# Kernel tuning notes

Measured on AMD Instinct MI355X. Metric: run time of the kernel, lower is better.

## Reference

```python
import jax, jax.numpy as jnp
import numpy as np

B, T, E = 2, 2048, 2048
H, HKV, DH = 16, 8, 128
G = H // HKV
WINDOW = 512
ROPE_THETA = 10000.0
EPS = 1e-6


def _rms_norm(x, w):
    # Gemma3RMSNorm: fp32 rms_norm with weight = 1 + w
    xf = x.astype(jnp.float32)
    y = xf * jax.lax.rsqrt(jnp.mean(xf * xf, axis=-1, keepdims=True) + EPS)
    return (y * (1.0 + w.astype(jnp.float32))).astype(x.dtype)


def _rotate_half(x):
    x1, x2 = x[..., : DH // 2], x[..., DH // 2 :]
    return jnp.concatenate((-x2, x1), axis=-1)


def setup_inputs() -> dict:
    key = jax.random.key(0)
    ks = jax.random.split(key, 5)
    s = 0.02
    return {
        "x": jax.random.normal(ks[0], (B, T, E), jnp.float32),
        "wq": jax.random.normal(ks[1], (H * DH, E), jnp.float32) * s,
        "wk": jax.random.normal(ks[2], (HKV * DH, E), jnp.float32) * s,
        "wv": jax.random.normal(ks[3], (HKV * DH, E), jnp.float32) * s,
        "wo": jax.random.normal(ks[4], (E, H * DH), jnp.float32) * s,
        "q_norm_w": jnp.zeros((DH,), jnp.float32),
        "k_norm_w": jnp.zeros((DH,), jnp.float32),
    }


def reference(x, wq, wk, wv, wo, q_norm_w, k_norm_w):
    # projections: [B,T,H,DH] -> [B,H,T,DH]
    q = (x @ wq.T).reshape(B, T, H, DH).transpose(0, 2, 1, 3)
    k = (x @ wk.T).reshape(B, T, HKV, DH).transpose(0, 2, 1, 3)
    v = (x @ wv.T).reshape(B, T, HKV, DH).transpose(0, 2, 1, 3)

    # QK-RMSNorm over head_dim
    q = _rms_norm(q, q_norm_w)
    k = _rms_norm(k, k_norm_w)

    # RoPE (prefill: positions 0..T-1)
    pos = jnp.arange(T, dtype=jnp.float32)
    inv_freq = 1.0 / (ROPE_THETA ** (jnp.arange(0, DH, 2, dtype=jnp.float32) / DH))
    freqs = pos[:, None] * inv_freq[None, :]          # [T, DH//2]
    emb = jnp.concatenate((freqs, freqs), axis=-1)    # [T, DH]
    cos = jnp.cos(emb)[None, None, :, :]
    sin = jnp.sin(emb)[None, None, :, :]
    q = q * cos + _rotate_half(q) * sin
    k = k * cos + _rotate_half(k) * sin

    # GQA attention with causal + sliding-window mask, fp32 scores
    q = q * (DH ** -0.5)
    qg = q.reshape(B, HKV, G, T, DH)
    att = jnp.einsum("bhgtd,bhkd->bhgtk", qg.astype(jnp.float32), k.astype(jnp.float32))

    dist = jnp.arange(T)[:, None] - jnp.arange(T)[None, :]   # [T, T]
    mask = (dist >= 0) & (dist <= WINDOW)
    att = jnp.where(mask[None, None, None, :, :], att, jnp.finfo(jnp.float32).min)
    att = jax.nn.softmax(att, axis=-1).astype(q.dtype)

    ctx = jnp.einsum("bhgtk,bhkd->bhgtd", att, v)
    out = ctx.reshape(B, H, T, DH).transpose(0, 2, 1, 3).reshape(B, T, H * DH)
    return out @ wo.T
```

## Files before the change

### kernel.cpp

```cpp
#include <hip/hip_runtime.h>
#include <hip/hip_bf16.h>
#include <stdint.h>

#define B_ 2
#define T_ 2048
#define E_ 2048
#define H_ 16
#define HKV_ 8
#define DH_ 128
#define WINDOW_ 512

typedef unsigned short ush;
typedef float f32x4 __attribute__((ext_vector_type(4)));
typedef __bf16 bf16x8 __attribute__((ext_vector_type(8)));
typedef uint32_t u32x4 __attribute__((ext_vector_type(4)));

static __device__ __forceinline__ ush f2bf(float f) {
    uint32_t u = __float_as_uint(f);
    uint32_t r = (u + 0x7fffu + ((u >> 16) & 1u)) >> 16;
    return (ush)r;
}
static __device__ __forceinline__ float bf2f(ush h) {
    return __uint_as_float(((uint32_t)h) << 16);
}

__global__ __launch_bounds__(256) void cast_all(const float* __restrict__ x,
        const float* __restrict__ wq, const float* __restrict__ wk,
        const float* __restrict__ wv, const float* __restrict__ wo,
        ush* __restrict__ dst) {
    const int stride = gridDim.x * blockDim.x;
    for (int i = blockIdx.x * blockDim.x + threadIdx.x; i < 5242880; i += stride) {
        const float4* src;
        if (i < 2097152)      src = (const float4*)x  + i;
        else if (i < 3145728) src = (const float4*)wq + (i - 2097152);
        else if (i < 3670016) src = (const float4*)wk + (i - 3145728);
        else if (i < 4194304) src = (const float4*)wv + (i - 3670016);
        else                  src = (const float4*)wo + (i - 4194304);
        const float4 f = *src;
        ushort4 o;
        o.x = f2bf(f.x); o.y = f2bf(f.y); o.z = f2bf(f.z); o.w = f2bf(f.w);
        reinterpret_cast<ushort4*>(dst)[i] = o;
    }
}

template <int MODE>
__global__ __launch_bounds__(512, 2) void gemm_bt3(
    const ush* __restrict__ A, const ush* __restrict__ Bm,
    float* __restrict__ Cf, ush* __restrict__ q, ush* __restrict__ k, ush* __restrict__ vT,
    int M, int N, int K)
{
    __shared__ ush As[3][128 * 64];
    __shared__ ush Bs[3][256 * 64];
    const int tid = threadIdx.x;
    const int lane = tid & 63;
    const int wid = tid >> 6;
    const int wr = wid >> 2, wc = wid & 3;
    const int g = lane >> 4, t = lane & 15;
    const int gm0 = blockIdx.x * 128, gn0 = blockIdx.y * 256;

    f32x4 acc[4][4] = {};

    auto stageA2 = [&](int kt, int m3) {
#pragma unroll
        for (int i = 0; i < 2; ++i) {
            const int C = i * 512 + tid;
            const int r = C >> 3, c = C & 7;
            const ush* src = A + (size_t)(gm0 + r) * K + (kt << 6) + ((c ^ (r & 7)) << 3);
            __builtin_amdgcn_global_load_lds(
                (const __attribute__((address_space(1))) void*)src,
                (__attribute__((address_space(3))) void*)(&As[m3][C << 3]), 16, 0, 0);
        }
    };
    auto stageB4 = [&](int kt, int m3) {
#pragma unroll
        for (int i = 0; i < 4; ++i) {
            const int C = i * 512 + tid;
            const int r = C >> 3, c = C & 7;
            const ush* src = Bm + (size_t)(gn0 + r) * K + (kt << 6) + ((c ^ (r & 7)) << 3);
            __builtin_amdgcn_global_load_lds(
                (const __attribute__((address_space(1))) void*)src,
                (__attribute__((address_space(3))) void*)(&Bs[m3][C << 3]), 16, 0, 0);
        }
    };

    const int nt = K >> 6;

    stageA2(0, 0); stageB4(0, 0);
    stageA2(1, 1); stageB4(1, 1);
    asm volatile("s_waitcnt vmcnt(6)" ::: "memory");
    __builtin_amdgcn_s_barrier();
    __builtin_amdgcn_sched_barrier(0);

    int m3 = 0;
    for (int kt = 0; kt < nt; ++kt) {
        const int st3 = (m3 + 2 >= 3) ? m3 - 1 : m3 + 2;
        bf16x8 af[4][2], bfr[4][2];

#pragma unroll
        for (int mf = 0; mf < 4; ++mf)
#pragma unroll
            for (int ks = 0; ks < 2; ++ks) {
                const int row = wr * 64 + mf * 16 + t;
                af[mf][ks] = *reinterpret_cast<const bf16x8*>(
                    &As[m3][row * 64 + ((((ks << 2) + g) ^ (t & 7)) << 3)]);
            }
#pragma unroll
        for (int nf = 0; nf < 4; ++nf)
#pragma unroll
            for (int ks = 0; ks < 2; ++ks) {
                const int row = wc * 64 + nf * 16 + t;
                bfr[nf][ks] = *reinterpret_cast<const bf16x8*>(
                    &Bs[m3][row * 64 + ((((ks << 2) + g) ^ (t & 7)) << 3)]);
            }

        if (kt + 2 < nt) { stageA2(kt + 2, st3); stageB4(kt + 2, st3); }

        __builtin_amdgcn_s_setprio(1);
#pragma unroll
        for (int ks = 0; ks < 2; ++ks)
#pragma unroll
            for (int mf = 0; mf < 4; ++mf)
#pragma unroll
                for (int nf = 0; nf < 4; ++nf)
                    acc[mf][nf] = __builtin_amdgcn_mfma_f32_16x16x32_bf16(
                        af[mf][ks], bfr[nf][ks], acc[mf][nf], 0, 0, 0);
        __builtin_amdgcn_s_setprio(0);

        if (kt + 1 < nt) {
            if (kt + 2 < nt) asm volatile("s_waitcnt vmcnt(6)" ::: "memory");
            else             asm volatile("s_waitcnt vmcnt(0)" ::: "memory");
        }
        __builtin_amdgcn_s_barrier();
        __builtin_amdgcn_sched_barrier(0);

        m3 = (m3 + 1 >= 3) ? 0 : m3 + 1;
    }

    const int rsub = (lane >> 4) << 2;
    const int csub = lane & 15;
#pragma unroll
    for (int mf = 0; mf < 4; ++mf) {
        const int row0 = gm0 + wr * 64 + mf * 16 + rsub;
#pragma unroll
        for (int nf = 0; nf < 4; ++nf) {
            const int col = gn0 + wc * 64 + nf * 16 + csub;
#pragma unroll
            for (int r = 0; r < 4; ++r) {
                const int row = row0 + r;
                if (MODE == 1) {
                    Cf[(size_t)row * N + col] = acc[mf][nf][r];
                } else {
                    const int bb = row >> 11, tt = row & (T_ - 1);
                    const ush val = f2bf(acc[mf][nf][r]);
                    if (col < H_ * DH_) {
                        const int hh = col >> 7, d = col & 127;
                        q[((((size_t)bb * H_ + hh) * T_ + tt) << 7) + d] = val;
                    } else if (col < H_ * DH_ + HKV_ * DH_) {
                        const int c2 = col - H_ * DH_;
                        const int hh = c2 >> 7, d = c2 & 127;
                        k[((((size_t)bb * HKV_ + hh) * T_ + tt) << 7) + d] = val;
                    } else {
                        const int c2 = col - H_ * DH_ - HKV_ * DH_;
                        const int hh = c2 >> 7, d = c2 & 127;
                        vT[((size_t)((bb * HKV_ + hh) * DH_ + d) << 11) + tt] = val;
                    }
                }
            }
        }
    }
}

__global__ __launch_bounds__(256) void norm_rope(ush* __restrict__ q, ush* __restrict__ k,
                                                 const float* __restrict__ qw,
                                                 const float* __restrict__ kw)
{
    const int lane = threadIdx.x & 63;
    const int row = blockIdx.x * 4 + (threadIdx.x >> 6);
    const int NQ = B_ * H_ * T_;
    ush* p; const float* w; int t; bool isq = (row < NQ);
    if (isq) { p = q + ((size_t)row << 7); t = row & (T_ - 1); w = qw; }
    else     { int r2 = row - NQ; p = k + ((size_t)r2 << 7); t = r2 & (T_ - 1); w = kw; }

    float x0 = bf2f(p[lane]);
    float x1 = bf2f(p[lane + 64]);
    float ss = x0 * x0 + x1 * x1;
#pragma unroll
    for (int off = 32; off; off >>= 1) ss += __shfl_xor(ss, off);
    const float rms = rsqrtf(ss * (1.0f / 128.0f) + 1e-6f);
    float y0 = x0 * rms * (1.0f + w[lane]);
    float y1 = x1 * rms * (1.0f + w[lane + 64]);

    const float invf = expf(-(float)lane * 0.14391156831212787f);
    const float fr = (float)t * invf;
    const float c = cosf(fr), s = sinf(fr);
    float o0 = y0 * c - y1 * s;
    float o1 = y1 * c + y0 * s;
    if (isq) { o0 *= 0.08838834764831845f; o1 *= 0.08838834764831845f; }
    p[lane] = f2bf(o0);
    p[lane + 64] = f2bf(o1);
}

__global__ __launch_bounds__(256) void attn_mfma(const ush* __restrict__ q,
        const ush* __restrict__ k, const ush* __restrict__ vT, ush* __restrict__ ctx)
{
    __shared__ ush Ks[2][32 * 128];
    __shared__ ush Vs[2][128 * 32];
    const int tid = threadIdx.x;
    const int lane = tid & 63;
    const int w = tid >> 6;
    const int g = lane >> 4;
    const int t = lane & 15;

    int bi = blockIdx.x;
    bi = (bi & 7) * 128 + (bi >> 3);
    const int qtile = bi & 31;
    const int hh = (bi >> 5) & 15;
    const int b = bi >> 9;
    const int qb = qtile * 64;
    const int hkv = hh >> 1;

    const ush* qptr = q + ((((size_t)b * H_ + hh) * T_ + qb) << 7);
    const ush* kbase = k + (((size_t)b * HKV_ + hkv) << 18);
    const ush* vtbase = vT + (((size_t)b * HKV_ + hkv) << 18);

    bf16x8 qf[4];
#pragma unroll
    for (int c = 0; c < 4; ++c)
        qf[c] = *reinterpret_cast<const bf16x8*>(qptr + ((16 * w + t) << 7) + 32 * c + 8 * g);

    const int kstart = (qb >= WINDOW_) ? (qb - WINDOW_) : 0;
    const int nt = (qb + 64 - kstart) >> 5;

    auto stage = [&](int ti, int buf) {
        const int kt0 = kstart + (ti << 5);
#pragma unroll
        for (int i = 0; i < 2; ++i) {
            const int C = w * 128 + i * 64 + lane;
            {
                const int row = C >> 4, ch = C & 15;
                const ush* gk = kbase + ((size_t)(kt0 + row) << 7) + ch * 8;
                __builtin_amdgcn_global_load_lds(
                    (const __attribute__((address_space(1))) void*)gk,
                    (__attribute__((address_space(3))) void*)(&Ks[buf][(w * 128 + i * 64) * 8]),
                    16, 0, 0);
            }
            {
                const int row = C >> 2, ch = C & 3;
                const ush* gv = vtbase + ((size_t)row << 11) + kt0 + ch * 8;
                __builtin_amdgcn_global_load_lds(
                    (const __attribute__((address_space(1))) void*)gv,
                    (__attribute__((address_space(3))) void*)(&Vs[buf][(w * 128 + i * 64) * 8]),
                    16, 0, 0);
            }
        }
    };

    float m = -1e30f, lsum = 0.f;
    f32x4 o[8] = {};

    stage(0, 0);
    __syncthreads();

    for (int ti = 0; ti < nt; ++ti) {
        const int cur = ti & 1;
        if (ti + 1 < nt) stage(ti + 1, cur ^ 1);
        const int kt0 = kstart + (ti << 5);
        const int qw0 = qb + 16 * w;
        const bool active = (kt0 + 31 >= qw0 - WINDOW_) && (kt0 <= qw0 + 15);
        if (active) {
            f32x4 st[2] = {};
#pragma unroll
            for (int s = 0; s < 2; ++s)
#pragma unroll
                for (int c = 0; c < 4; ++c) {
                    bf16x8 kf = *reinterpret_cast<const bf16x8*>(
                        &Ks[cur][(16 * s + t) * 128 + 32 * c + 8 * g]);
                    st[s] = __builtin_amdgcn_mfma_f32_16x16x32_bf16(kf, qf[c], st[s], 0, 0, 0);
                }
            const int tg = qb + 16 * w + t;
            float e[2][4];
            float mymax = -3e38f;
#pragma unroll
            for (int s = 0; s < 2; ++s)
#pragma unroll
                for (int r = 0; r < 4; ++r) {
                    const int key = kt0 + 16 * s + 4 * g + r;
                    const int dist = tg - key;
                    const bool valid = (dist >= 0) && (dist <= WINDOW_);
                    const float sv = valid ? st[s][r] : -3e38f;
                    e[s][r] = sv;
                    mymax = fmaxf(mymax, sv);
                }
            mymax = fmaxf(mymax, __shfl_xor(mymax, 16));
            mymax = fmaxf(mymax, __shfl_xor(mymax, 32));
            const float mn = fmaxf(m, mymax);
            const float sc = __expf(m - mn);
            float esum = 0.f;
#pragma unroll
            for (int s = 0; s < 2; ++s)
#pragma unroll
                for (int r = 0; r < 4; ++r) {
                    const float ev = __expf(e[s][r] - mn);
                    e[s][r] = ev;
                    esum += ev;
                }
            esum += __shfl_xor(esum, 16);
            esum += __shfl_xor(esum, 32);
            lsum = lsum * sc + esum;
            m = mn;
#pragma unroll
            for (int ds = 0; ds < 8; ++ds) {
                o[ds][0] *= sc; o[ds][1] *= sc; o[ds][2] *= sc; o[ds][3] *= sc;
            }
            uint32_t word[2][2];
#pragma unroll
            for (int s = 0; s < 2; ++s)
#pragma unroll
                for (int wd = 0; wd < 2; ++wd)
                    word[s][wd] = (uint32_t)f2bf(e[s][2 * wd])
                                | ((uint32_t)f2bf(e[s][2 * wd + 1]) << 16);
            u32x4 bw;
#pragma unroll
            for (int e2 = 0; e2 < 4; ++e2) {
                const int srcl = 16 * (2 * (g & 1) + (e2 >> 1)) + t;
                const uint32_t v0 = __shfl(word[0][e2 & 1], srcl);
                const uint32_t v1 = __shfl(word[1][e2 & 1], srcl);
                bw[e2] = (g >= 2) ? v1 : v0;
            }
            const bf16x8 pF = __builtin_bit_cast(bf16x8, bw);
#pragma unroll
            for (int ds = 0; ds < 8; ++ds) {
                bf16x8 vtF = *reinterpret_cast<const bf16x8*>(
                    &Vs[cur][(16 * ds + t) * 32 + 8 * g]);
                o[ds] = __builtin_amdgcn_mfma_f32_16x16x32_bf16(vtF, pF, o[ds], 0, 0, 0);
            }
        }
        __syncthreads();
    }

    const float linv = 1.0f / lsum;
    ush* cptr = ctx + (((size_t)b * T_ + qb + 16 * w + t) * (H_ * DH_)) + hh * DH_;
#pragma unroll
    for (int ds = 0; ds < 8; ++ds) {
        ushort4 pk;
        pk.x = f2bf(o[ds][0] * linv);
        pk.y = f2bf(o[ds][1] * linv);
        pk.z = f2bf(o[ds][2] * linv);
        pk.w = f2bf(o[ds][3] * linv);
        *reinterpret_cast<ushort4*>(cptr + 16 * ds + 4 * g) = pk;
    }
}

extern "C" void kernel_launch(void* const* d_in, const int* in_sizes, int n_in,
                              void* d_out, int out_size, void* d_ws, size_t ws_size,
                              hipStream_t stream)
{
    const float* x   = (const float*)d_in[0];
    const float* wq  = (const float*)d_in[1];
    const float* wk  = (const float*)d_in[2];
    const float* wv  = (const float*)d_in[3];
    const float* wo  = (const float*)d_in[4];
    const float* qnw = (const float*)d_in[5];
    const float* knw = (const float*)d_in[6];
    float* out = (float*)d_out;

    ush* ws    = (ush*)d_ws;
    ush* xbf   = ws;
    ush* wqkv  = xbf  + 8388608;
    ush* wobf  = wqkv + 8388608;
    ush* qraw  = wobf + 4194304;
    ush* kraw  = qraw + 8388608;
    ush* vTb   = kraw + 4194304;
    ush* ctx   = vTb  + 4194304;

    cast_all<<<2048, 256, 0, stream>>>(x, wq, wk, wv, wo, ws);

    gemm_bt3<0><<<dim3(32, 16), 512, 0, stream>>>(xbf, wqkv, nullptr, qraw, kraw, vTb,
                                                  4096, 4096, 2048);
    norm_rope<<<(65536 + 32768) / 4, 256, 0, stream>>>(qraw, kraw, qnw, knw);
    attn_mfma<<<1024, 256, 0, stream>>>(qraw, kraw, vTb, ctx);
    gemm_bt3<1><<<dim3(32, 8), 512, 0, stream>>>(ctx, wobf, out, nullptr, nullptr, nullptr,
                                                 4096, 2048, 2048);
    (void)in_sizes; (void)n_in; (void)out_size; (void)ws_size;
}
```

Baseline: 236.8 us.

## Switch GEMMs to 32x32x16 MFMA with BK=32 and 4-stage pipeline

Rewrites the bf16 GEMM kernel to use 32x32x16 MFMA instructions with a K-step of 32, a four-buffer LDS ring (three stages in flight), and a new XOR swizzle. The QKV projection now uses 256x256 block tiles (M_REP=4), half as many blocks, while the output projection keeps 128x256. The goal is fewer LDS reads per MFMA and more reuse per block, at the cost of more accumulator registers and a longer, more intricate vmcnt wait schedule.

```diff
diff --git a/kernel.cpp b/kernel.cpp
--- a/kernel.cpp
+++ b/kernel.cpp
@@ -12,6 +12,7 @@
 
 typedef unsigned short ush;
 typedef float f32x4 __attribute__((ext_vector_type(4)));
+typedef float f32x16 __attribute__((ext_vector_type(16)));
 typedef __bf16 bf16x8 __attribute__((ext_vector_type(8)));
 typedef uint32_t u32x4 __attribute__((ext_vector_type(4)));
 
@@ -43,115 +44,118 @@
     }
 }
 
-template <int MODE>
-__global__ __launch_bounds__(512, 2) void gemm_bt3(
+template <int M_REP, int MODE>
+__global__ __launch_bounds__(512, 2) void gemm_bt4(
     const ush* __restrict__ A, const ush* __restrict__ Bm,
     float* __restrict__ Cf, ush* __restrict__ q, ush* __restrict__ k, ush* __restrict__ vT,
     int M, int N, int K)
 {
-    __shared__ ush As[3][128 * 64];
-    __shared__ ush Bs[3][256 * 64];
+    __shared__ ush As[4][M_REP * 64 * 32];
+    __shared__ ush Bs[4][256 * 32];
     const int tid = threadIdx.x;
     const int lane = tid & 63;
     const int wid = tid >> 6;
     const int wr = wid >> 2, wc = wid & 3;
-    const int g = lane >> 4, t = lane & 15;
-    const int gm0 = blockIdx.x * 128, gn0 = blockIdx.y * 256;
-
-    f32x4 acc[4][4] = {};
-
-    auto stageA2 = [&](int kt, int m3) {
+    const int l31 = lane & 31, lh = lane >> 5;
+    const int gm0 = blockIdx.x * (M_REP * 64), gn0 = blockIdx.y * 256;
+
+    f32x16 acc[M_REP][2] = {};
+
+    auto stage = [&](int kt, int buf) {
+#pragma unroll
+        for (int i = 0; i < M_REP / 2; ++i) {
+            const int C = i * 512 + tid;
+            const int r = C >> 2, c = C & 3;
+            const ush* src = A + (size_t)(gm0 + r) * K + (kt << 5)
+                             + ((c ^ ((r >> 1) & 3)) << 3);
+            __builtin_amdgcn_global_load_lds(
+                (const __attribute__((address_space(1))) void*)src,
+                (__attribute__((address_space(3))) void*)(&As[buf][C << 3]), 16, 0, 0);
+        }
 #pragma unroll
         for (int i = 0; i < 2; ++i) {
             const int C = i * 512 + tid;
-            const int r = C >> 3, c = C & 7;
-            const ush* src = A + (size_t)(gm0 + r) * K + (kt << 6) + ((c ^ (r & 7)) << 3);
+            const int r = C >> 2, c = C & 3;
+            const ush* src = Bm + (size_t)(gn0 + r) * K + (kt << 5)
+                             + ((c ^ ((r >> 1) & 3)) << 3);
             __builtin_amdgcn_global_load_lds(
                 (const __attribute__((address_space(1))) void*)src,
-                (__attribute__((address_space(3))) void*)(&As[m3][C << 3]), 16, 0, 0);
+                (__attribute__((address_space(3))) void*)(&Bs[buf][C << 3]), 16, 0, 0);
         }
     };
-    auto stageB4 = [&](int kt, int m3) {
-#pragma unroll
-        for (int i = 0; i < 4; ++i) {
-            const int C = i * 512 + tid;
-            const int r = C >> 3, c = C & 7;
-            const ush* src = Bm + (size_t)(gn0 + r) * K + (kt << 6) + ((c ^ (r & 7)) << 3);
-            __builtin_amdgcn_global_load_lds(
-                (const __attribute__((address_space(1))) void*)src,
-                (__attribute__((address_space(3))) void*)(&Bs[m3][C << 3]), 16, 0, 0);
-        }
-    };
-
-    const int nt = K >> 6;
-
-    stageA2(0, 0); stageB4(0, 0);
-    stageA2(1, 1); stageB4(1, 1);
-    asm volatile("s_waitcnt vmcnt(6)" ::: "memory");
+
+    const int nt = K >> 5;
+
+    stage(0, 0); stage(1, 1); stage(2, 2);
+    if constexpr (M_REP == 4) asm volatile("s_waitcnt vmcnt(8)" ::: "memory");
+    else                      asm volatile("s_waitcnt vmcnt(6)" ::: "memory");
     __builtin_amdgcn_s_barrier();
     __builtin_amdgcn_sched_barrier(0);
 
-    int m3 = 0;
-    for (int kt = 0; kt < nt; ++kt) {
-        const int st3 = (m3 + 2 >= 3) ? m3 - 1 : m3 + 2;
-        bf16x8 af[4][2], bfr[4][2];
-
-#pragma unroll
-        for (int mf = 0; mf < 4; ++mf)
-#pragma unroll
-            for (int ks = 0; ks < 2; ++ks) {
-                const int row = wr * 64 + mf * 16 + t;
+    for (int t = 0; t < nt; ++t) {
+        const int buf = t & 3;
+        bf16x8 af[M_REP][2], bfr[2][2];
+
+#pragma unroll
+        for (int mf = 0; mf < M_REP; ++mf) {
+            const int row = wr * (M_REP * 32) + mf * 32 + l31;
+            const int sw = (row >> 1) & 3;
+#pragma unroll
+            for (int ks = 0; ks < 2; ++ks)
                 af[mf][ks] = *reinterpret_cast<const bf16x8*>(
-                    &As[m3][row * 64 + ((((ks << 2) + g) ^ (t & 7)) << 3)]);
-            }
-#pragma unroll
-        for (int nf = 0; nf < 4; ++nf)
-#pragma unroll
-            for (int ks = 0; ks < 2; ++ks) {
-                const int row = wc * 64 + nf * 16 + t;
+                    &As[buf][row * 32 + (((ks * 2 + lh) ^ sw) << 3)]);
+        }
+#pragma unroll
+        for (int nf = 0; nf < 2; ++nf) {
+            const int row = wc * 64 + nf * 32 + l31;
+            const int sw = (row >> 1) & 3;
+#pragma unroll
+            for (int ks = 0; ks < 2; ++ks)
                 bfr[nf][ks] = *reinterpret_cast<const bf16x8*>(
-                    &Bs[m3][row * 64 + ((((ks << 2) + g) ^ (t & 7)) << 3)]);
-            }
-
-        if (kt + 2 < nt) { stageA2(kt + 2, st3); stageB4(kt + 2, st3); }
+                    &Bs[buf][row * 32 + (((ks * 2 + lh) ^ sw) << 3)]);
+        }
+
+        if (t + 3 < nt) stage(t + 3, (t + 3) & 3);
 
         __builtin_amdgcn_s_setprio(1);
 #pragma unroll
         for (int ks = 0; ks < 2; ++ks)
 #pragma unroll
-            for (int mf = 0; mf < 4; ++mf)
-#pragma unroll
-                for (int nf = 0; nf < 4; ++nf)
-                    acc[mf][nf] = __builtin_amdgcn_mfma_f32_16x16x32_bf16(
+            for (int mf = 0; mf < M_REP; ++mf)
+#pragma unroll
+                for (int nf = 0; nf < 2; ++nf)
+                    acc[mf][nf] = __builtin_amdgcn_mfma_f32_32x32x16_bf16(
                         af[mf][ks], bfr[nf][ks], acc[mf][nf], 0, 0, 0);
         __builtin_amdgcn_s_setprio(0);
 
-        if (kt + 1 < nt) {
-            if (kt + 2 < nt) asm volatile("s_waitcnt vmcnt(6)" ::: "memory");
-            else             asm volatile("s_waitcnt vmcnt(0)" ::: "memory");
+        if (t + 3 < nt) {
+            if constexpr (M_REP == 4) asm volatile("s_waitcnt vmcnt(8)" ::: "memory");
+            else                      asm volatile("s_waitcnt vmcnt(6)" ::: "memory");
+        } else if (t + 2 < nt) {
+            if constexpr (M_REP == 4) asm volatile("s_waitcnt vmcnt(4)" ::: "memory");
+            else                      asm volatile("s_waitcnt vmcnt(3)" ::: "memory");
+        } else if (t + 1 < nt) {
+            asm volatile("s_waitcnt vmcnt(0)" ::: "memory");
         }
         __builtin_amdgcn_s_barrier();
         __builtin_amdgcn_sched_barrier(0);
-
-        m3 = (m3 + 1 >= 3) ? 0 : m3 + 1;
-    }
-
-    const int rsub = (lane >> 4) << 2;
-    const int csub = lane & 15;
-#pragma unroll
-    for (int mf = 0; mf < 4; ++mf) {
-        const int row0 = gm0 + wr * 64 + mf * 16 + rsub;
-#pragma unroll
-        for (int nf = 0; nf < 4; ++nf) {
-            const int col = gn0 + wc * 64 + nf * 16 + csub;
-#pragma unroll
-            for (int r = 0; r < 4; ++r) {
-                const int row = row0 + r;
+    }
+
+#pragma unroll
+    for (int mf = 0; mf < M_REP; ++mf) {
+        const int rbase = gm0 + wr * (M_REP * 32) + mf * 32 + 4 * lh;
+#pragma unroll
+        for (int nf = 0; nf < 2; ++nf) {
+            const int col = gn0 + wc * 64 + nf * 32 + l31;
+#pragma unroll
+            for (int r = 0; r < 16; ++r) {
+                const int row = rbase + (r & 3) + 8 * (r >> 2);
+                const float v = acc[mf][nf][r];
                 if (MODE == 1) {
-                    Cf[(size_t)row * N + col] = acc[mf][nf][r];
+                    Cf[(size_t)row * N + col] = v;
                 } else {
                     const int bb = row >> 11, tt = row & (T_ - 1);
-                    const ush val = f2bf(acc[mf][nf][r]);
+                    const ush val = f2bf(v);
                     if (col < H_ * DH_) {
                         const int hh = col >> 7, d = col & 127;
                         q[((((size_t)bb * H_ + hh) * T_ + tt) << 7) + d] = val;
@@ -375,11 +379,11 @@
 
     cast_all<<<2048, 256, 0, stream>>>(x, wq, wk, wv, wo, ws);
 
-    gemm_bt3<0><<<dim3(32, 16), 512, 0, stream>>>(xbf, wqkv, nullptr, qraw, kraw, vTb,
-                                                  4096, 4096, 2048);
+    gemm_bt4<4, 0><<<dim3(16, 16), 512, 0, stream>>>(xbf, wqkv, nullptr, qraw, kraw, vTb,
+                                                     4096, 4096, 2048);
     norm_rope<<<(65536 + 32768) / 4, 256, 0, stream>>>(qraw, kraw, qnw, knw);
     attn_mfma<<<1024, 256, 0, stream>>>(qraw, kraw, vTb, ctx);
-    gemm_bt3<1><<<dim3(32, 8), 512, 0, stream>>>(ctx, wobf, out, nullptr, nullptr, nullptr,
-                                                 4096, 2048, 2048);
+    gemm_bt4<2, 1><<<dim3(32, 8), 512, 0, stream>>>(ctx, wobf, out, nullptr, nullptr, nullptr,
+                                                    4096, 2048, 2048);
     (void)in_sizes; (void)n_in; (void)out_size; (void)ws_size;
 }
```

New measurement: 248.2 us. 4.8% more time.

## Replace triple-buffered GEMM with double-buffered ping-pong phases and larger QKV tile

Applied to the files above, without the earlier changes.

Rewrites the bf16 GEMM to use two LDS buffers instead of three. The main loop is split into phases over pairs of M-fragments, with barriers between phases so waves interleave LDS reads and MFMA work. The tile height becomes a template parameter: the QKV projection uses 256x256 tiles (half as many blocks) and the output projection keeps 128x256. The aim is better operand reuse and a schedule closer to the hipBLASLt ping-pong style. In exchange it exposes more load latency because only one tile is prefetched, and it adds extra barriers.

```diff
diff --git a/kernel.cpp b/kernel.cpp
--- a/kernel.cpp
+++ b/kernel.cpp
@@ -43,35 +43,36 @@
     }
 }
 
-template <int MODE>
-__global__ __launch_bounds__(512, 2) void gemm_bt3(
+template <int MF, int MODE>
+__global__ __launch_bounds__(512, 2) void gemm_bt5(
     const ush* __restrict__ A, const ush* __restrict__ Bm,
     float* __restrict__ Cf, ush* __restrict__ q, ush* __restrict__ k, ush* __restrict__ vT,
     int M, int N, int K)
 {
-    __shared__ ush As[3][128 * 64];
-    __shared__ ush Bs[3][256 * 64];
+    constexpr int BM = MF * 32;
+    __shared__ ush As[2][BM * 64];
+    __shared__ ush Bs[2][256 * 64];
     const int tid = threadIdx.x;
     const int lane = tid & 63;
     const int wid = tid >> 6;
     const int wr = wid >> 2, wc = wid & 3;
     const int g = lane >> 4, t = lane & 15;
-    const int gm0 = blockIdx.x * 128, gn0 = blockIdx.y * 256;
-
-    f32x4 acc[4][4] = {};
-
-    auto stageA2 = [&](int kt, int m3) {
-#pragma unroll
-        for (int i = 0; i < 2; ++i) {
+    const int gm0 = blockIdx.x * BM, gn0 = blockIdx.y * 256;
+
+    f32x4 acc[MF][4] = {};
+
+    auto stageA = [&](int kt, int buf) {
+#pragma unroll
+        for (int i = 0; i < BM / 64; ++i) {
             const int C = i * 512 + tid;
             const int r = C >> 3, c = C & 7;
             const ush* src = A + (size_t)(gm0 + r) * K + (kt << 6) + ((c ^ (r & 7)) << 3);
             __builtin_amdgcn_global_load_lds(
                 (const __attribute__((address_space(1))) void*)src,
-                (__attribute__((address_space(3))) void*)(&As[m3][C << 3]), 16, 0, 0);
+                (__attribute__((address_space(3))) void*)(&As[buf][C << 3]), 16, 0, 0);
         }
     };
-    auto stageB4 = [&](int kt, int m3) {
+    auto stageB = [&](int kt, int buf) {
 #pragma unroll
         for (int i = 0; i < 4; ++i) {
             const int C = i * 512 + tid;
@@ -79,68 +80,66 @@
             const ush* src = Bm + (size_t)(gn0 + r) * K + (kt << 6) + ((c ^ (r & 7)) << 3);
             __builtin_amdgcn_global_load_lds(
                 (const __attribute__((address_space(1))) void*)src,
-                (__attribute__((address_space(3))) void*)(&Bs[m3][C << 3]), 16, 0, 0);
+                (__attribute__((address_space(3))) void*)(&Bs[buf][C << 3]), 16, 0, 0);
         }
     };
 
     const int nt = K >> 6;
 
-    stageA2(0, 0); stageB4(0, 0);
-    stageA2(1, 1); stageB4(1, 1);
-    asm volatile("s_waitcnt vmcnt(6)" ::: "memory");
+    stageA(0, 0); stageB(0, 0);
+    asm volatile("s_waitcnt vmcnt(0)" ::: "memory");
     __builtin_amdgcn_s_barrier();
     __builtin_amdgcn_sched_barrier(0);
 
-    int m3 = 0;
     for (int kt = 0; kt < nt; ++kt) {
-        const int st3 = (m3 + 2 >= 3) ? m3 - 1 : m3 + 2;
-        bf16x8 af[4][2], bfr[4][2];
-
-#pragma unroll
-        for (int mf = 0; mf < 4; ++mf)
-#pragma unroll
-            for (int ks = 0; ks < 2; ++ks) {
-                const int row = wr * 64 + mf * 16 + t;
-                af[mf][ks] = *reinterpret_cast<const bf16x8*>(
-                    &As[m3][row * 64 + ((((ks << 2) + g) ^ (t & 7)) << 3)]);
-            }
-#pragma unroll
-        for (int nf = 0; nf < 4; ++nf)
-#pragma unroll
-            for (int ks = 0; ks < 2; ++ks) {
-                const int row = wc * 64 + nf * 16 + t;
-                bfr[nf][ks] = *reinterpret_cast<const bf16x8*>(
-                    &Bs[m3][row * 64 + ((((ks << 2) + g) ^ (t & 7)) << 3)]);
-            }
-
-        if (kt + 2 < nt) { stageA2(kt + 2, st3); stageB4(kt + 2, st3); }
-
-        __builtin_amdgcn_s_setprio(1);
-#pragma unroll
-        for (int ks = 0; ks < 2; ++ks)
-#pragma unroll
-            for (int mf = 0; mf < 4; ++mf)
+        const int cur = kt & 1;
+        bf16x8 bfr[4][2];
+
+#pragma unroll
+        for (int p = 0; p < MF / 2; ++p) {
+            bf16x8 af[2][2];
+#pragma unroll
+            for (int mm = 0; mm < 2; ++mm)
+#pragma unroll
+                for (int ks = 0; ks < 2; ++ks) {
+                    const int row = wr * (MF * 16) + (2 * p + mm) * 16 + t;
+                    af[mm][ks] = *reinterpret_cast<const bf16x8*>(
+                        &As[cur][row * 64 + ((((ks << 2) + g) ^ (t & 7)) << 3)]);
+                }
+            if (p == 0) {
 #pragma unroll
                 for (int nf = 0; nf < 4; ++nf)
-                    acc[mf][nf] = __builtin_amdgcn_mfma_f32_16x16x32_bf16(
-                        af[mf][ks], bfr[nf][ks], acc[mf][nf], 0, 0, 0);
-        __builtin_amdgcn_s_setprio(0);
-
-        if (kt + 1 < nt) {
-            if (kt + 2 < nt) asm volatile("s_waitcnt vmcnt(6)" ::: "memory");
-            else             asm volatile("s_waitcnt vmcnt(0)" ::: "memory");
-        }
-        __builtin_amdgcn_s_barrier();
-        __builtin_amdgcn_sched_barrier(0);
-
-        m3 = (m3 + 1 >= 3) ? 0 : m3 + 1;
+#pragma unroll
+                    for (int ks = 0; ks < 2; ++ks) {
+                        const int row = wc * 64 + nf * 16 + t;
+                        bfr[nf][ks] = *reinterpret_cast<const bf16x8*>(
+                            &Bs[cur][row * 64 + ((((ks << 2) + g) ^ (t & 7)) << 3)]);
+                    }
+                if (kt + 1 < nt) { stageA(kt + 1, cur ^ 1); stageB(kt + 1, cur ^ 1); }
+            }
+            __builtin_amdgcn_s_barrier();
+            __builtin_amdgcn_s_setprio(1);
+#pragma unroll
+            for (int ks = 0; ks < 2; ++ks)
+#pragma unroll
+                for (int mm = 0; mm < 2; ++mm)
+#pragma unroll
+                    for (int nf = 0; nf < 4; ++nf)
+                        acc[2 * p + mm][nf] = __builtin_amdgcn_mfma_f32_16x16x32_bf16(
+                            af[mm][ks], bfr[nf][ks], acc[2 * p + mm][nf], 0, 0, 0);
+            __builtin_amdgcn_s_setprio(0);
+            if (p == MF / 2 - 1 && kt + 1 < nt)
+                asm volatile("s_waitcnt vmcnt(0)" ::: "memory");
+            __builtin_amdgcn_s_barrier();
+            __builtin_amdgcn_sched_barrier(0);
+        }
     }
 
     const int rsub = (lane >> 4) << 2;
     const int csub = lane & 15;
 #pragma unroll
-    for (int mf = 0; mf < 4; ++mf) {
-        const int row0 = gm0 + wr * 64 + mf * 16 + rsub;
+    for (int mf = 0; mf < MF; ++mf) {
+        const int row0 = gm0 + wr * (MF * 16) + mf * 16 + rsub;
 #pragma unroll
         for (int nf = 0; nf < 4; ++nf) {
             const int col = gn0 + wc * 64 + nf * 16 + csub;
@@ -375,11 +374,11 @@
 
     cast_all<<<2048, 256, 0, stream>>>(x, wq, wk, wv, wo, ws);
 
-    gemm_bt3<0><<<dim3(32, 16), 512, 0, stream>>>(xbf, wqkv, nullptr, qraw, kraw, vTb,
-                                                  4096, 4096, 2048);
+    gemm_bt5<8, 0><<<dim3(16, 16), 512, 0, stream>>>(xbf, wqkv, nullptr, qraw, kraw, vTb,
+                                                     4096, 4096, 2048);
     norm_rope<<<(65536 + 32768) / 4, 256, 0, stream>>>(qraw, kraw, qnw, knw);
     attn_mfma<<<1024, 256, 0, stream>>>(qraw, kraw, vTb, ctx);
-    gemm_bt3<1><<<dim3(32, 8), 512, 0, stream>>>(ctx, wobf, out, nullptr, nullptr, nullptr,
-                                                 4096, 2048, 2048);
+    gemm_bt5<4, 1><<<dim3(32, 8), 512, 0, stream>>>(ctx, wobf, out, nullptr, nullptr, nullptr,
+                                                    4096, 2048, 2048);
     (void)in_sizes; (void)n_in; (void)out_size; (void)ws_size;
 }
```

Measured after the change: 236.0 us. About the same (-0.3%).

## Shrink GEMM tiles to 128x128 with double buffering and swizzled block order

Applied to the files above, without the earlier changes.

The GEMM kernel changes from 128x256 tiles with a 3-stage LDS pipeline to 128x128 tiles with 2-stage double buffering. Launch bounds now allow 4 blocks per CU, and a block-index swizzle groups tiles for L2 reuse. The aim is more blocks in flight and better occupancy on the CUs, at the cost of less data reuse per tile, a shallower prefetch pipeline and a full vmcnt(0) wait every iteration.

```diff
diff --git a/kernel.cpp b/kernel.cpp
--- a/kernel.cpp
+++ b/kernel.cpp
@@ -44,23 +44,28 @@
 }
 
 template <int MODE>
-__global__ __launch_bounds__(512, 2) void gemm_bt3(
+__global__ __launch_bounds__(512, 4) void gemm_bt6(
     const ush* __restrict__ A, const ush* __restrict__ Bm,
     float* __restrict__ Cf, ush* __restrict__ q, ush* __restrict__ k, ush* __restrict__ vT,
     int M, int N, int K)
 {
-    __shared__ ush As[3][128 * 64];
-    __shared__ ush Bs[3][256 * 64];
+    __shared__ ush As[2][128 * 64];
+    __shared__ ush Bs[2][128 * 64];
     const int tid = threadIdx.x;
     const int lane = tid & 63;
     const int wid = tid >> 6;
-    const int wr = wid >> 2, wc = wid & 3;
+    const int wr = wid >> 1, wc = wid & 1;
     const int g = lane >> 4, t = lane & 15;
-    const int gm0 = blockIdx.x * 128, gn0 = blockIdx.y * 256;
-
-    f32x4 acc[4][4] = {};
-
-    auto stageA2 = [&](int kt, int m3) {
+
+    const int nwg = gridDim.x * gridDim.y;
+    const int r0 = blockIdx.y * gridDim.x + blockIdx.x;
+    const int swz = (r0 & 7) * (nwg >> 3) + (r0 >> 3);
+    const int gm0 = (swz & 31) * 128;
+    const int gn0 = (swz >> 5) * 128;
+
+    f32x4 acc[2][4] = {};
+
+    auto stage = [&](int kt, int buf) {
 #pragma unroll
         for (int i = 0; i < 2; ++i) {
             const int C = i * 512 + tid;
@@ -68,41 +73,39 @@
             const ush* src = A + (size_t)(gm0 + r) * K + (kt << 6) + ((c ^ (r & 7)) << 3);
             __builtin_amdgcn_global_load_lds(
                 (const __attribute__((address_space(1))) void*)src,
-                (__attribute__((address_space(3))) void*)(&As[m3][C << 3]), 16, 0, 0);
-        }
-    };
-    auto stageB4 = [&](int kt, int m3) {
-#pragma unroll
-        for (int i = 0; i < 4; ++i) {
+                (__attribute__((address_space(3))) void*)(&As[buf][C << 3]), 16, 0, 0);
+        }
+#pragma unroll
+        for (int i = 0; i < 2; ++i) {
             const int C = i * 512 + tid;
             const int r = C >> 3, c = C & 7;
             const ush* src = Bm + (size_t)(gn0 + r) * K + (kt << 6) + ((c ^ (r & 7)) << 3);
             __builtin_amdgcn_global_load_lds(
                 (const __attribute__((address_space(1))) void*)src,
-                (__attribute__((address_space(3))) void*)(&Bs[m3][C << 3]), 16, 0, 0);
+                (__attribute__((address_space(3))) void*)(&Bs[buf][C << 3]), 16, 0, 0);
         }
     };
 
     const int nt = K >> 6;
 
-    stageA2(0, 0); stageB4(0, 0);
-    stageA2(1, 1); stageB4(1, 1);
-    asm volatile("s_waitcnt vmcnt(6)" ::: "memory");
+    stage(0, 0);
+    asm volatile("s_waitcnt vmcnt(0)" ::: "memory");
     __builtin_amdgcn_s_barrier();
     __builtin_amdgcn_sched_barrier(0);
 
-    int m3 = 0;
     for (int kt = 0; kt < nt; ++kt) {
-        const int st3 = (m3 + 2 >= 3) ? m3 - 1 : m3 + 2;
-        bf16x8 af[4][2], bfr[4][2];
-
-#pragma unroll
-        for (int mf = 0; mf < 4; ++mf)
+        const int buf = kt & 1;
+
+        if (kt + 1 < nt) stage(kt + 1, buf ^ 1);
+
+        bf16x8 af[2][2], bfr[4][2];
+#pragma unroll
+        for (int mf = 0; mf < 2; ++mf)
 #pragma unroll
             for (int ks = 0; ks < 2; ++ks) {
-                const int row = wr * 64 + mf * 16 + t;
+                const int row = wr * 32 + mf * 16 + t;
                 af[mf][ks] = *reinterpret_cast<const bf16x8*>(
-                    &As[m3][row * 64 + ((((ks << 2) + g) ^ (t & 7)) << 3)]);
+                    &As[buf][row * 64 + ((((ks << 2) + g) ^ (t & 7)) << 3)]);
             }
 #pragma unroll
         for (int nf = 0; nf < 4; ++nf)
@@ -110,37 +113,31 @@
             for (int ks = 0; ks < 2; ++ks) {
                 const int row = wc * 64 + nf * 16 + t;
                 bfr[nf][ks] = *reinterpret_cast<const bf16x8*>(
-                    &Bs[m3][row * 64 + ((((ks << 2) + g) ^ (t & 7)) << 3)]);
-            }
-
-        if (kt + 2 < nt) { stageA2(kt + 2, st3); stageB4(kt + 2, st3); }
+                    &Bs[buf][row * 64 + ((((ks << 2) + g) ^ (t & 7)) << 3)]);
+            }
 
         __builtin_amdgcn_s_setprio(1);
 #pragma unroll
         for (int ks = 0; ks < 2; ++ks)
 #pragma unroll
-            for (int mf = 0; mf < 4; ++mf)
+            for (int mf = 0; mf < 2; ++mf)
 #pragma unroll
                 for (int nf = 0; nf < 4; ++nf)
                     acc[mf][nf] = __builtin_amdgcn_mfma_f32_16x16x32_bf16(
                         af[mf][ks], bfr[nf][ks], acc[mf][nf], 0, 0, 0);
         __builtin_amdgcn_s_setprio(0);
 
-        if (kt + 1 < nt) {
-            if (kt + 2 < nt) asm volatile("s_waitcnt vmcnt(6)" ::: "memory");
-            else             asm volatile("s_waitcnt vmcnt(0)" ::: "memory");
-        }
+        if (kt + 1 < nt)
+            asm volatile("s_waitcnt vmcnt(0)" ::: "memory");
         __builtin_amdgcn_s_barrier();
         __builtin_amdgcn_sched_barrier(0);
-
-        m3 = (m3 + 1 >= 3) ? 0 : m3 + 1;
     }
 
     const int rsub = (lane >> 4) << 2;
     const int csub = lane & 15;
 #pragma unroll
-    for (int mf = 0; mf < 4; ++mf) {
-        const int row0 = gm0 + wr * 64 + mf * 16 + rsub;
+    for (int mf = 0; mf < 2; ++mf) {
+        const int row0 = gm0 + wr * 32 + mf * 16 + rsub;
 #pragma unroll
         for (int nf = 0; nf < 4; ++nf) {
             const int col = gn0 + wc * 64 + nf * 16 + csub;
@@ -375,11 +372,11 @@
 
     cast_all<<<2048, 256, 0, stream>>>(x, wq, wk, wv, wo, ws);
 
-    gemm_bt3<0><<<dim3(32, 16), 512, 0, stream>>>(xbf, wqkv, nullptr, qraw, kraw, vTb,
+    gemm_bt6<0><<<dim3(32, 32), 512, 0, stream>>>(xbf, wqkv, nullptr, qraw, kraw, vTb,
                                                   4096, 4096, 2048);
     norm_rope<<<(65536 + 32768) / 4, 256, 0, stream>>>(qraw, kraw, qnw, knw);
     attn_mfma<<<1024, 256, 0, stream>>>(qraw, kraw, vTb, ctx);
-    gemm_bt3<1><<<dim3(32, 8), 512, 0, stream>>>(ctx, wobf, out, nullptr, nullptr, nullptr,
-                                                 4096, 2048, 2048);
+    gemm_bt6<1><<<dim3(32, 16), 512, 0, stream>>>(ctx, wobf, out, nullptr, nullptr, nullptr,
+                                                  4096, 2048, 2048);
     (void)in_sizes; (void)n_in; (void)out_size; (void)ws_size;
 }
```

Result: no change. 239.9 us (+1.3%).
